# Performance work log

Hardware: AMD Instinct MI355X
Metric: run time of the kernel (lower is better)

Reference implementation:

```python
import jax, jax.numpy as jnp
import numpy as np
import math

EMBED = 1024
FF = 4096
HEADS = 16
HEAD = EMBED // HEADS
EPS = 1e-5


def new_gelu(x):
    c = math.sqrt(2.0 / math.pi)
    return 0.5 * x * (1.0 + jnp.tanh(c * (x + 0.044715 * x ** 3)))


def layer_norm(x, g, b):
    mu = jnp.mean(x, axis=-1, keepdims=True)
    var = jnp.var(x, axis=-1, keepdims=True)
    return (x - mu) * jax.lax.rsqrt(var + EPS) * g + b


def setup_inputs() -> dict:
    key = jax.random.key(0)
    ks = jax.random.split(key, 16)
    s = 0.02
    d = {
        'x': jax.random.normal(ks[0], (2, 2048, EMBED), jnp.float32),
        'Wq': jax.random.normal(ks[1], (EMBED, EMBED)) * s,
        'bq': jnp.zeros((EMBED,)),
        'Wk': jax.random.normal(ks[2], (EMBED, EMBED)) * s,
        'bk': jnp.zeros((EMBED,)),
        'Wv': jax.random.normal(ks[3], (EMBED, EMBED)) * s,
        'bv': jnp.zeros((EMBED,)),
        'Wp': jax.random.normal(ks[4], (EMBED, EMBED)) * s,
        'bp': jnp.zeros((EMBED,)),
        'W1': jax.random.normal(ks[5], (EMBED, FF)) * s,
        'b1': jnp.zeros((FF,)),
        'W2': jax.random.normal(ks[6], (FF, EMBED)) * s,
        'b2': jnp.zeros((EMBED,)),
        'g1': jnp.ones((EMBED,)), 'be1': jnp.zeros((EMBED,)),
        'g2': jnp.ones((EMBED,)), 'be2': jnp.zeros((EMBED,)),
    }
    return d


def reference(x, Wq, bq, Wk, bk, Wv, bv, Wp, bp, W1, b1, W2, b2, g1, be1, g2, be2):
    B, S, D = x.shape
    h = layer_norm(x, g1, be1)
    # project and split heads: [B,S,D] -> [B,H,S,Hd]
    def heads(y):
        return y.reshape(B, S, HEADS, HEAD).transpose(0, 2, 1, 3)
    Q = heads(h @ Wq + bq)
    K = heads(h @ Wk + bk)
    V = heads(h @ Wv + bv)
    att = jnp.einsum('bhqd,bhkd->bhqk', Q, K) / math.sqrt(HEAD)
    att = jax.nn.softmax(att, axis=-1)
    out = jnp.einsum('bhqk,bhkd->bhqd', att, V)
    out = out.transpose(0, 2, 1, 3).reshape(B, S, D)
    x = x + (out @ Wp + bp)  # dropout p=0 / eval -> identity
    h2 = layer_norm(x, g2, be2)
    x = x + (new_gelu(h2 @ W1 + b1) @ W2 + b2)
    return x
```

## Files before the change

kernel.cpp:

```cpp
#include <hip/hip_runtime.h>
#include <cstdint>


typedef __attribute__((ext_vector_type(8))) short short8;
typedef __attribute__((ext_vector_type(4))) float f32x4;

#define QSCL 0.18033688011112042f

__device__ __forceinline__ float bf2f(unsigned short u) {
    union { unsigned int i; float f; } v; v.i = ((unsigned int)u) << 16; return v.f;
}
__device__ __forceinline__ unsigned short f2bf(float f) {
    union { float f; unsigned int i; } v; v.f = f;
    unsigned int u = v.i;
    u += 0x7fff + ((u >> 16) & 1);
    return (unsigned short)(u >> 16);
}
__device__ __forceinline__ float gelu_f(float x) {
    float u = 0.7978845608028654f * (x + 0.044715f * x * x * x);
    float t = 1.f - 2.f / (__expf(2.f * u) + 1.f);
    return 0.5f * x * (1.f + t);
}

__device__ __forceinline__ void ln_dev(
    const float* __restrict__ x, const float* __restrict__ g,
    const float* __restrict__ b, unsigned short* __restrict__ o,
    int row, float* red)
{
    const int tid = threadIdx.x;
    const float4 v = ((const float4*)(x + (size_t)row * 1024))[tid];
    float f0 = v.x, f1 = v.y, f2 = v.z, f3 = v.w;
    float sum = f0 + f1 + f2 + f3;
    float sq  = f0 * f0 + f1 * f1 + f2 * f2 + f3 * f3;
    for (int off = 1; off < 64; off <<= 1) {
        sum += __shfl_xor(sum, off);
        sq  += __shfl_xor(sq,  off);
    }
    int wv = tid >> 6, ln = tid & 63;
    if (ln == 0) { red[wv] = sum; red[4 + wv] = sq; }
    __syncthreads();
    sum = red[0] + red[1] + red[2] + red[3];
    sq  = red[4] + red[5] + red[6] + red[7];
    float mu  = sum * (1.0f / 1024.0f);
    float var = sq  * (1.0f / 1024.0f) - mu * mu;
    float rsd = rsqrtf(fmaxf(var, 0.f) + 1e-5f);
    const float4 gg = ((const float4*)g)[tid];
    const float4 bb = ((const float4*)b)[tid];
    unsigned short* orow = o + (size_t)row * 1024;
    orow[4 * tid + 0] = f2bf((f0 - mu) * rsd * gg.x + bb.x);
    orow[4 * tid + 1] = f2bf((f1 - mu) * rsd * gg.y + bb.y);
    orow[4 * tid + 2] = f2bf((f2 - mu) * rsd * gg.z + bb.z);
    orow[4 * tid + 3] = f2bf((f3 - mu) * rsd * gg.w + bb.w);
}

__device__ __forceinline__ void transpose_dev(
    const float* __restrict__ in, unsigned short* __restrict__ out,
    int R, int C, int inStride, int bx, int by, unsigned short* tile ,
    float scale)
{
    const int tx = threadIdx.x & 15, ty = threadIdx.x >> 4;
    const int c0 = bx * 64, r0 = by * 64;
#pragma unroll
    for (int i = 0; i < 4; ++i) {
        int r = ty + 16 * i;
        float4 v = *(const float4*)(in + (size_t)(r0 + r) * inStride + c0 + tx * 4);
        tile[r * 70 + tx * 4 + 0] = f2bf(v.x * scale);
        tile[r * 70 + tx * 4 + 1] = f2bf(v.y * scale);
        tile[r * 70 + tx * 4 + 2] = f2bf(v.z * scale);
        tile[r * 70 + tx * 4 + 3] = f2bf(v.w * scale);
    }
    __syncthreads();
#pragma unroll
    for (int i = 0; i < 4; ++i) {
        int c = ty * 4 + i;
        ushort4 o;
        o.x = tile[(tx * 4 + 0) * 70 + c];
        o.y = tile[(tx * 4 + 1) * 70 + c];
        o.z = tile[(tx * 4 + 2) * 70 + c];
        o.w = tile[(tx * 4 + 3) * 70 + c];
        *(ushort4*)(out + (size_t)(c0 + c) * R + r0 + tx * 4) = o;
    }
}

__global__ __launch_bounds__(256) void ln_k(
    const float* __restrict__ x, const float* __restrict__ g,
    const float* __restrict__ b, unsigned short* __restrict__ o)
{
    __shared__ float red[8];
    ln_dev(x, g, b, o, blockIdx.x, red);
}
__global__ __launch_bounds__(256) void transpose_f2b(
    const float* __restrict__ in, unsigned short* __restrict__ out,
    int R, int C, int inStride, float scale)
{
    __shared__ unsigned short tile[64 * 70];
    transpose_dev(in, out, R, C, inStride, blockIdx.x, blockIdx.y, tile, scale);
}

__global__ __launch_bounds__(256) void prep1_k(
    const float* __restrict__ x,
    const float* __restrict__ g1, const float* __restrict__ be1,
    const float* __restrict__ Wq, const float* __restrict__ Wk,
    const float* __restrict__ Wv,
    const float* __restrict__ bq, const float* __restrict__ bk,
    const float* __restrict__ bv,
    unsigned short* __restrict__ hb,
    unsigned short* __restrict__ WTqkv,
    float* __restrict__ bcat)
{
    __shared__ unsigned short smem[64 * 70];
    const int b = blockIdx.x;
    if (b < 4096) {
        ln_dev(x, g1, be1, hb, b, (float*)smem);
    } else if (b < 4096 + 768) {
        int t = b - 4096;
        int w = t >> 8;
        int tt = t & 255;
        const float* W = (w == 0) ? Wq : (w == 1) ? Wk : Wv;
        transpose_dev(W, WTqkv + (size_t)w * 1024 * 1024,
                      1024, 1024, 1024, tt & 15, tt >> 4, smem,
                      (w == 0) ? QSCL : 1.f);
    } else {
        int i = (b - 4096 - 768) * 256 + threadIdx.x;
        float v = (i < 1024) ? bq[i] * QSCL : (i < 2048) ? bk[i - 1024] : bv[i - 2048];
        bcat[i] = v;
    }
}

__global__ __launch_bounds__(256) void prep2_k(
    const float* __restrict__ x1,
    const float* __restrict__ g2, const float* __restrict__ be2,
    const float* __restrict__ W1, const float* __restrict__ W2,
    unsigned short* __restrict__ h2,
    unsigned short* __restrict__ WT1,
    unsigned short* __restrict__ WT2)
{
    __shared__ unsigned short smem[64 * 70];
    const int b = blockIdx.x;
    if (b < 4096) {
        ln_dev(x1, g2, be2, h2, b, (float*)smem);
    } else if (b < 4096 + 1024) {
        int t = b - 4096;
        transpose_dev(W1, WT1, 1024, 4096, 4096, t & 63, t >> 6, smem, 1.f);
    } else {
        int t = b - 4096 - 1024;
        transpose_dev(W2, WT2, 4096, 1024, 1024, t & 15, t >> 4, smem, 1.f);
    }
}

__global__ __launch_bounds__(256) void vt_k(
    const unsigned short* __restrict__ src, int stride,
    unsigned short* __restrict__ Vt)
{
    __shared__ unsigned short tile[64][70];
    const int tx = threadIdx.x & 15, ty = threadIdx.x >> 4;
    const int t0 = blockIdx.x * 64;
    const int bh = blockIdx.y;
    const int bo = (bh >> 4) * 2048;
    const int ho = (bh & 15) * 64;
    const unsigned short* s = src + (size_t)bo * stride + ho;
#pragma unroll
    for (int i = 0; i < 4; ++i) {
        int r = ty + 16 * i;
        ushort4 v = *(const ushort4*)(s + (size_t)(t0 + r) * stride + tx * 4);
        tile[r][tx * 4 + 0] = v.x;
        tile[r][tx * 4 + 1] = v.y;
        tile[r][tx * 4 + 2] = v.z;
        tile[r][tx * 4 + 3] = v.w;
    }
    __syncthreads();
    unsigned short* dst = Vt + (size_t)bh * 64 * 2048;
    const int hh = tx >> 3;
    const int uu = (tx & 7) * 2;
#pragma unroll
    for (int i = 0; i < 4; ++i) {
        int d = ty * 4 + i;
        ushort4 o;
        o.x = tile[32 * hh + uu][d];
        o.y = tile[32 * hh + 16 + uu][d];
        o.z = tile[32 * hh + uu + 1][d];
        o.w = tile[32 * hh + 17 + uu][d];
        *(ushort4*)(dst + (size_t)d * 2048 + t0 + tx * 4) = o;
    }
}

__global__ __launch_bounds__(256, 3) void gemm6(
    const unsigned short* __restrict__ A,
    const unsigned short* __restrict__ Bt,
    const float* __restrict__ bias,
    const float* __restrict__ res,
    void* __restrict__ C,
    int M, int N, int K, int ldb, int dogelu, int out32, float bscale)
{
    __shared__ unsigned short sA[2][128 * 34];
    __shared__ unsigned short sB[2][128 * 34];
    const int tid  = threadIdx.x;
    const int wave = tid >> 6;
    const int lane = tid & 63;
    const int quad = lane >> 4;
    const int l15  = lane & 15;
    const int bm = blockIdx.y * 128;
    const int bn = blockIdx.x * 128;
    const int wM = (wave & 1) * 64;
    const int wN = (wave >> 1) * 64;

    f32x4 acc[4][4];
#pragma unroll
    for (int i = 0; i < 4; ++i)
#pragma unroll
        for (int j = 0; j < 4; ++j)
            acc[i][j] = (f32x4){0.f, 0.f, 0.f, 0.f};

    const int rowS = tid >> 2;
    const int kcS  = (tid & 3) * 8;
    const unsigned short* gA  = A  + (size_t)(bm + rowS) * K + kcS;
    const unsigned short* gA2 = gA + (size_t)64 * K;
    const unsigned short* gB  = Bt + (size_t)(bn + rowS) * ldb + kcS;
    const unsigned short* gB2 = gB + (size_t)64 * ldb;
    const int lo1 = rowS * 34 + kcS;
    const int lo2 = (rowS + 64) * 34 + kcS;

    const int np = K >> 5;
    *(short8*)(&sA[0][lo1]) = *(const short8*)(gA);
    *(short8*)(&sA[0][lo2]) = *(const short8*)(gA2);
    *(short8*)(&sB[0][lo1]) = *(const short8*)(gB);
    *(short8*)(&sB[0][lo2]) = *(const short8*)(gB2);
    short8 ar1 = *(const short8*)(gA + 32);
    short8 ar2 = *(const short8*)(gA2 + 32);
    short8 br1 = *(const short8*)(gB + 32);
    short8 br2 = *(const short8*)(gB2 + 32);

    for (int p = 0; p < np; ++p) {
        const int buf = p & 1;
        __syncthreads();

        short8 aF[4], bF[4];
#pragma unroll
        for (int mi = 0; mi < 4; ++mi)
            aF[mi] = *(const short8*)(&sA[buf][(wM + mi * 16 + l15) * 34 + quad * 8]);
#pragma unroll
        for (int ni = 0; ni < 4; ++ni)
            bF[ni] = *(const short8*)(&sB[buf][(wN + ni * 16 + l15) * 34 + quad * 8]);

        if (p + 1 < np) {
            *(short8*)(&sA[buf ^ 1][lo1]) = ar1;
            *(short8*)(&sA[buf ^ 1][lo2]) = ar2;
            *(short8*)(&sB[buf ^ 1][lo1]) = br1;
            *(short8*)(&sB[buf ^ 1][lo2]) = br2;
            if (p + 2 < np) {
                const int k2 = (p + 2) << 5;
                ar1 = *(const short8*)(gA + k2);
                ar2 = *(const short8*)(gA2 + k2);
                br1 = *(const short8*)(gB + k2);
                br2 = *(const short8*)(gB2 + k2);
            }
        }

        __builtin_amdgcn_s_setprio(1);
#pragma unroll
        for (int mi = 0; mi < 4; ++mi)
#pragma unroll
            for (int ni = 0; ni < 4; ++ni)
                acc[mi][ni] = __builtin_amdgcn_mfma_f32_16x16x32_bf16(
                    aF[mi], bF[ni], acc[mi][ni], 0, 0, 0);
        __builtin_amdgcn_s_setprio(0);
    }

#pragma unroll
    for (int ni = 0; ni < 4; ++ni) {
        int col = bn + wN + ni * 16 + l15;
        float bv = bias ? bias[col] * bscale : 0.f;
#pragma unroll
        for (int mi = 0; mi < 4; ++mi) {
            int row = bm + wM + mi * 16 + quad * 4;
#pragma unroll
            for (int r = 0; r < 4; ++r) {
                float v = acc[mi][ni][r] + bv;
                if (dogelu) v = gelu_f(v);
                size_t idx = (size_t)(row + r) * N + col;
                if (res) v += res[idx];
                if (out32) ((float*)C)[idx] = v;
                else       ((unsigned short*)C)[idx] = f2bf(v);
            }
        }
    }
}

__global__ __launch_bounds__(512, 4) void gemm5(
    const unsigned short* __restrict__ A,
    const unsigned short* __restrict__ Bt,
    const float* __restrict__ bias,
    const float* __restrict__ res,
    void* __restrict__ C,
    int M, int N, int K, int ldb, int dogelu, int out32, float bscale)
{
    __shared__ unsigned short sA[2][128 * 68];
    __shared__ unsigned short sB[2][128 * 68];
    const int tid  = threadIdx.x;
    const int wave = tid >> 6;
    const int lane = tid & 63;
    const int quad = lane >> 4;
    const int l15  = lane & 15;
    const int bm = blockIdx.y * 128;
    const int bn = blockIdx.x * 128;
    const int wM = (wave & 1) * 64;
    const int wN = (wave >> 1) * 32;

    f32x4 acc[4][2];
#pragma unroll
    for (int i = 0; i < 4; ++i)
#pragma unroll
        for (int j = 0; j < 2; ++j)
            acc[i][j] = (f32x4){0.f, 0.f, 0.f, 0.f};

    const int rowS = tid >> 3;
    const int kcS  = (tid & 7) * 8;
    const unsigned short* gA  = A  + (size_t)(bm + rowS) * K + kcS;
    const unsigned short* gA2 = gA + (size_t)64 * K;
    const unsigned short* gB  = Bt + (size_t)(bn + rowS) * ldb + kcS;
    const unsigned short* gB2 = gB + (size_t)64 * ldb;
    const int lo1 = rowS * 68 + kcS;
    const int lo2 = (rowS + 64) * 68 + kcS;

    const int nt = K >> 6;
    *(short8*)(&sA[0][lo1]) = *(const short8*)(gA);
    *(short8*)(&sA[0][lo2]) = *(const short8*)(gA2);
    *(short8*)(&sB[0][lo1]) = *(const short8*)(gB);
    *(short8*)(&sB[0][lo2]) = *(const short8*)(gB2);
    short8 ar1 = *(const short8*)(gA + 64);
    short8 ar2 = *(const short8*)(gA2 + 64);
    short8 br1 = *(const short8*)(gB + 64);
    short8 br2 = *(const short8*)(gB2 + 64);

    for (int t = 0; t < nt; ++t) {
        const int buf = t & 1;
        __syncthreads();

        short8 aF[4], bF[2];
#pragma unroll
        for (int mi = 0; mi < 4; ++mi)
            aF[mi] = *(const short8*)(&sA[buf][(wM + mi * 16 + l15) * 68 + quad * 8]);
#pragma unroll
        for (int ni = 0; ni < 2; ++ni)
            bF[ni] = *(const short8*)(&sB[buf][(wN + ni * 16 + l15) * 68 + quad * 8]);

        if (t + 1 < nt) {
            *(short8*)(&sA[buf ^ 1][lo1]) = ar1;
            *(short8*)(&sA[buf ^ 1][lo2]) = ar2;
            *(short8*)(&sB[buf ^ 1][lo1]) = br1;
            *(short8*)(&sB[buf ^ 1][lo2]) = br2;
            if (t + 2 < nt) {
                const int k2 = (t + 2) << 6;
                ar1 = *(const short8*)(gA + k2);
                ar2 = *(const short8*)(gA2 + k2);
                br1 = *(const short8*)(gB + k2);
                br2 = *(const short8*)(gB2 + k2);
            }
        }

        __builtin_amdgcn_s_setprio(1);
#pragma unroll
        for (int mi = 0; mi < 4; ++mi)
#pragma unroll
            for (int ni = 0; ni < 2; ++ni)
                acc[mi][ni] = __builtin_amdgcn_mfma_f32_16x16x32_bf16(
                    aF[mi], bF[ni], acc[mi][ni], 0, 0, 0);
        __builtin_amdgcn_s_setprio(0);

#pragma unroll
        for (int mi = 0; mi < 4; ++mi)
            aF[mi] = *(const short8*)(&sA[buf][(wM + mi * 16 + l15) * 68 + 32 + quad * 8]);
#pragma unroll
        for (int ni = 0; ni < 2; ++ni)
            bF[ni] = *(const short8*)(&sB[buf][(wN + ni * 16 + l15) * 68 + 32 + quad * 8]);

        __builtin_amdgcn_s_setprio(1);
#pragma unroll
        for (int mi = 0; mi < 4; ++mi)
#pragma unroll
            for (int ni = 0; ni < 2; ++ni)
                acc[mi][ni] = __builtin_amdgcn_mfma_f32_16x16x32_bf16(
                    aF[mi], bF[ni], acc[mi][ni], 0, 0, 0);
        __builtin_amdgcn_s_setprio(0);
    }

#pragma unroll
    for (int ni = 0; ni < 2; ++ni) {
        int col = bn + wN + ni * 16 + l15;
        float bv = bias ? bias[col] * bscale : 0.f;
#pragma unroll
        for (int mi = 0; mi < 4; ++mi) {
            int row = bm + wM + mi * 16 + quad * 4;
#pragma unroll
            for (int r = 0; r < 4; ++r) {
                float v = acc[mi][ni][r] + bv;
                if (dogelu) v = gelu_f(v);
                size_t idx = (size_t)(row + r) * N + col;
                if (res) v += res[idx];
                if (out32) ((float*)C)[idx] = v;
                else       ((unsigned short*)C)[idx] = f2bf(v);
            }
        }
    }
}

__global__ __launch_bounds__(512, 1) void attn_k(
    const unsigned short* __restrict__ Q,
    const unsigned short* __restrict__ K,
    const unsigned short* __restrict__ Vt,
    unsigned short* __restrict__ O, int qs)
{
    __shared__ unsigned short smem[67584];
    unsigned short* sK = smem;
    unsigned short* sV = smem + 4 * 5632;
    unsigned short* sP = smem + 8 * 5632;

    const int tid  = threadIdx.x;
    const int wave = tid >> 6;
    const int g    = wave & 3;
    const int h    = wave >> 2;
    const int lane = tid & 63;
    const int quad = lane >> 4;
    const int l15  = lane & 15;
    const int bh = blockIdx.x * 4 + (blockIdx.y & 3);
    const int qb = (blockIdx.y >> 2) * 256;
    const int bo = (bh >> 4) * 2048;
    const int ho = (bh & 15) * 64;

    const unsigned short* Qb  = Q  + (size_t)bo * qs + ho;
    const unsigned short* Kb  = K  + (size_t)bo * qs + ho;
    const unsigned short* Vtb = Vt + (size_t)bh * 64 * 2048;
    unsigned short* sPg = sP + g * 5632;
    const int ni0 = 2 * h;

    short8 qF[2][4];
#pragma unroll
    for (int ks = 0; ks < 2; ++ks)
#pragma unroll
        for (int mi = 0; mi < 4; ++mi)
            qF[ks][mi] = *(const short8*)(Qb +
                (size_t)(qb + g * 64 + mi * 16 + l15) * qs + ks * 32 + quad * 8);

    short8 onesF;
#pragma unroll
    for (int j = 0; j < 8; ++j) onesF[j] = (short)0x3F80;

    f32x4 accO[4][4];
    f32x4 accL[4];
#pragma unroll
    for (int mi = 0; mi < 4; ++mi) {
        accL[mi] = (f32x4){0.f, 0.f, 0.f, 0.f};
#pragma unroll
        for (int nd = 0; nd < 4; ++nd) accO[mi][nd] = (f32x4){0.f, 0.f, 0.f, 0.f};
    }

    const int rowS = tid >> 3;
    const int dcS  = (tid & 7) * 8;

    short8 kr[2], vr[2];
#pragma unroll
    for (int s = 0; s < 2; ++s) {
        kr[s] = *(const short8*)(Kb + (size_t)(s * 64 + rowS) * qs + dcS);
        vr[s] = *(const short8*)(Vtb + (size_t)rowS * 2048 + s * 64 + dcS);
    }
#pragma unroll
    for (int s = 0; s < 2; ++s) {
        *(short8*)(sK + s * 5632 + rowS * 88 + dcS) = kr[s];
        *(short8*)(sV + s * 5632 + rowS * 88 + dcS) = vr[s];
    }
#pragma unroll
    for (int s = 0; s < 2; ++s) {
        kr[s] = *(const short8*)(Kb + (size_t)(128 + s * 64 + rowS) * qs + dcS);
        vr[s] = *(const short8*)(Vtb + (size_t)rowS * 2048 + 128 + s * 64 + dcS);
    }

    for (int kt = 0; kt < 2048; kt += 128) {
        const int buf = (kt >> 7) & 1;
        __syncthreads();

#pragma unroll
        for (int s = 0; s < 2; ++s) {
            const unsigned short* sKb = sK + (buf * 2 + s) * 5632;
            const unsigned short* sVb = sV + (buf * 2 + s) * 5632;

            short8 bK[2][2];
#pragma unroll
            for (int ks = 0; ks < 2; ++ks)
#pragma unroll
                for (int nj = 0; nj < 2; ++nj)
                    bK[ks][nj] = *(const short8*)(sKb +
                        ((ni0 + nj) * 16 + l15) * 88 + ks * 32 + quad * 8);

            f32x4 s0[4], s1[4];
#pragma unroll
            for (int mi = 0; mi < 4; ++mi) {
                s0[mi] = (f32x4){0.f, 0.f, 0.f, 0.f};
                s1[mi] = s0[mi];
#pragma unroll
                for (int ks = 0; ks < 2; ++ks) {
                    s0[mi] = __builtin_amdgcn_mfma_f32_16x16x32_bf16(qF[ks][mi], bK[ks][0], s0[mi], 0, 0, 0);
                    s1[mi] = __builtin_amdgcn_mfma_f32_16x16x32_bf16(qF[ks][mi], bK[ks][1], s1[mi], 0, 0, 0);
                }
            }

            if (s == 0 && kt + 128 < 2048) {
#pragma unroll
                for (int u = 0; u < 2; ++u) {
                    *(short8*)(sK + ((buf ^ 1) * 2 + u) * 5632 + rowS * 88 + dcS) = kr[u];
                    *(short8*)(sV + ((buf ^ 1) * 2 + u) * 5632 + rowS * 88 + dcS) = vr[u];
                }
                if (kt + 256 < 2048) {
#pragma unroll
                    for (int u = 0; u < 2; ++u) {
                        kr[u] = *(const short8*)(Kb + (size_t)(kt + 256 + u * 64 + rowS) * qs + dcS);
                        vr[u] = *(const short8*)(Vtb + (size_t)rowS * 2048 + kt + 256 + u * 64 + dcS);
                    }
                }
            }

#pragma unroll
            for (int mi = 0; mi < 4; ++mi)
#pragma unroll
                for (int r = 0; r < 4; ++r) {
                    float p0 = __builtin_amdgcn_exp2f(s0[mi][r]);
                    float p1 = __builtin_amdgcn_exp2f(s1[mi][r]);
                    unsigned int w;
                    asm("v_cvt_pk_bf16_f32 %0, %1, %2" : "=v"(w) : "v"(p0), "v"(p1));
                    *(unsigned int*)(sPg + (mi * 16 + quad * 4 + r) * 88 + h * 32 + l15 * 2) = w;
                }

            short8 aP[4], bV[4];
#pragma unroll
            for (int nd = 0; nd < 4; ++nd)
                bV[nd] = *(const short8*)(sVb + (nd * 16 + l15) * 88 + h * 32 + quad * 8);
#pragma unroll
            for (int mi = 0; mi < 4; ++mi)
                aP[mi] = *(const short8*)(sPg + (mi * 16 + l15) * 88 + h * 32 + quad * 8);

            __builtin_amdgcn_s_setprio(1);
#pragma unroll
            for (int mi = 0; mi < 4; ++mi) {
#pragma unroll
                for (int nd = 0; nd < 4; ++nd)
                    accO[mi][nd] = __builtin_amdgcn_mfma_f32_16x16x32_bf16(
                        aP[mi], bV[nd], accO[mi][nd], 0, 0, 0);
                accL[mi] = __builtin_amdgcn_mfma_f32_16x16x32_bf16(
                    aP[mi], onesF, accL[mi], 0, 0, 0);
            }
            __builtin_amdgcn_s_setprio(0);
        }
    }

    __syncthreads();
    float* scr = (float*)smem;
    float* po = scr + (size_t)(g * 64 + lane) * 68;
    float* pl = scr + 17408 + (size_t)(g * 64 + lane) * 20;
    if (h == 1) {
#pragma unroll
        for (int mi = 0; mi < 4; ++mi) {
#pragma unroll
            for (int nd = 0; nd < 4; ++nd)
                *(f32x4*)(po + mi * 16 + nd * 4) = accO[mi][nd];
            *(f32x4*)(pl + mi * 4) = accL[mi];
        }
    }
    __syncthreads();
    if (h == 0) {
#pragma unroll
        for (int mi = 0; mi < 4; ++mi) {
            accL[mi] += *(const f32x4*)(pl + mi * 4);
#pragma unroll
            for (int nd = 0; nd < 4; ++nd)
                accO[mi][nd] += *(const f32x4*)(po + mi * 16 + nd * 4);
        }
#pragma unroll
        for (int mi = 0; mi < 4; ++mi)
#pragma unroll
            for (int r = 0; r < 4; ++r) {
                int row = qb + g * 64 + mi * 16 + quad * 4 + r;
                float inv = 1.f / accL[mi][r];
#pragma unroll
                for (int nd = 0; nd < 4; ++nd)
                    O[(size_t)(bo + row) * 1024 + ho + nd * 16 + l15] =
                        f2bf(accO[mi][nd][r] * inv);
            }
    }
}

extern "C" void kernel_launch(void* const* d_in, const int* in_sizes, int n_in,
                              void* d_out, int out_size, void* d_ws, size_t ws_size,
                              hipStream_t stream)
{
    (void)in_sizes; (void)n_in; (void)out_size;
    const float* x   = (const float*)d_in[0];
    const float* Wq  = (const float*)d_in[1];
    const float* bq  = (const float*)d_in[2];
    const float* Wk  = (const float*)d_in[3];
    const float* bk  = (const float*)d_in[4];
    const float* Wv  = (const float*)d_in[5];
    const float* bv  = (const float*)d_in[6];
    const float* Wp  = (const float*)d_in[7];
    const float* bp  = (const float*)d_in[8];
    const float* W1  = (const float*)d_in[9];
    const float* b1  = (const float*)d_in[10];
    const float* W2  = (const float*)d_in[11];
    const float* b2  = (const float*)d_in[12];
    const float* g1  = (const float*)d_in[13];
    const float* be1 = (const float*)d_in[14];
    const float* g2  = (const float*)d_in[15];
    const float* be2 = (const float*)d_in[16];
    float* out = (float*)d_out;

    char* ws = (char*)d_ws;
    char* dob = (char*)d_out;
    const size_t MB = 1024 * 1024;

    if (ws_size >= 40 * MB) {
        unsigned short* hb    = (unsigned short*)dob;
        unsigned short* WTqkv = (unsigned short*)(dob + 8 * MB);
        float*          bcat  = (float*)(dob + 14 * MB);
        unsigned short* QKV   = (unsigned short*)ws;
        unsigned short* att   = (unsigned short*)(ws + 24 * MB);
        unsigned short* Vt    = (unsigned short*)(ws + 32 * MB);
        unsigned short* WTp   = (unsigned short*)(ws + 32 * MB);
        unsigned short* h2    = (unsigned short*)ws;
        unsigned short* WT1   = (unsigned short*)(ws + 8 * MB);
        unsigned short* WT2   = (unsigned short*)(ws + 16 * MB);
        unsigned short* act   = (unsigned short*)(ws + 24 * MB);

        prep1_k<<<4096 + 768 + 12, 256, 0, stream>>>(
            x, g1, be1, Wq, Wk, Wv, bq, bk, bv, hb, WTqkv, bcat);
        gemm6<<<dim3(24, 32), 256, 0, stream>>>(hb, WTqkv, bcat, nullptr, QKV,
                                                4096, 3072, 1024, 1024, 0, 0, 1.f);
        vt_k<<<dim3(32, 32), 256, 0, stream>>>(QKV + 2048, 3072, Vt);
        attn_k<<<dim3(8, 32), 512, 0, stream>>>(QKV, QKV + 1024, Vt, att, 3072);
        transpose_f2b<<<dim3(16, 16), 256, 0, stream>>>(Wp, WTp, 1024, 1024, 1024, 1.f);
        gemm5<<<dim3(8, 32), 512, 0, stream>>>(att, WTp, bp, x, out,
                                               4096, 1024, 1024, 1024, 0, 1, 1.f);
        prep2_k<<<4096 + 2048, 256, 0, stream>>>(out, g2, be2, W1, W2, h2, WT1, WT2);
        for (int c = 0; c < 2; ++c) {
            gemm6<<<dim3(16, 32), 256, 0, stream>>>(h2, WT1 + (size_t)c * 2048 * 1024,
                                                    b1 + c * 2048, nullptr, act,
                                                    4096, 2048, 1024, 1024, 1, 0, 1.f);
            gemm5<<<dim3(8, 32), 512, 0, stream>>>(act, WT2 + (size_t)c * 2048,
                                                   c == 0 ? b2 : nullptr, out, out,
                                                   4096, 1024, 2048, 4096, 0, 1, 1.f);
        }
    } else {
        unsigned short* Qw  = (unsigned short*)(ws);
        unsigned short* Kw  = (unsigned short*)(ws + 8 * MB);
        unsigned short* Vw  = (unsigned short*)(ws + 16 * MB);
        unsigned short* hb  = (unsigned short*)dob;
        unsigned short* WTq = (unsigned short*)(dob + 8 * MB);
        unsigned short* VtF = (unsigned short*)(dob + 8 * MB);
        unsigned short* att = Qw;
        unsigned short* WTb = Kw;
        unsigned short* h2  = Vw;
        unsigned short* act = Qw;

        ln_k<<<4096, 256, 0, stream>>>(x, g1, be1, hb);
        transpose_f2b<<<dim3(16, 16), 256, 0, stream>>>(Wq, WTq, 1024, 1024, 1024, QSCL);
        gemm5<<<dim3(8, 32), 512, 0, stream>>>(hb, WTq, bq, nullptr, Qw, 4096, 1024, 1024, 1024, 0, 0, QSCL);
        transpose_f2b<<<dim3(16, 16), 256, 0, stream>>>(Wk, WTq, 1024, 1024, 1024, 1.f);
        gemm5<<<dim3(8, 32), 512, 0, stream>>>(hb, WTq, bk, nullptr, Kw, 4096, 1024, 1024, 1024, 0, 0, 1.f);
        transpose_f2b<<<dim3(16, 16), 256, 0, stream>>>(Wv, WTq, 1024, 1024, 1024, 1.f);
        gemm5<<<dim3(8, 32), 512, 0, stream>>>(hb, WTq, bv, nullptr, Vw, 4096, 1024, 1024, 1024, 0, 0, 1.f);
        vt_k<<<dim3(32, 32), 256, 0, stream>>>(Vw, 1024, VtF);
        attn_k<<<dim3(8, 32), 512, 0, stream>>>(Qw, Kw, VtF, att, 1024);
        transpose_f2b<<<dim3(16, 16), 256, 0, stream>>>(Wp, WTb, 1024, 1024, 1024, 1.f);
        gemm5<<<dim3(8, 32), 512, 0, stream>>>(att, WTb, bp, x, out, 4096, 1024, 1024, 1024, 0, 1, 1.f);
        ln_k<<<4096, 256, 0, stream>>>(out, g2, be2, h2);
        for (int c = 0; c < 4; ++c) {
            transpose_f2b<<<dim3(16, 16), 256, 0, stream>>>(W1 + c * 1024, WTb, 1024, 1024, 4096, 1.f);
            gemm5<<<dim3(8, 32), 512, 0, stream>>>(h2, WTb, b1 + c * 1024, nullptr, act,
                                                   4096, 1024, 1024, 1024, 1, 0, 1.f);
            unsigned short* WT2c = WTb + 1024 * 1024;
            transpose_f2b<<<dim3(16, 16), 256, 0, stream>>>(W2 + (size_t)c * 1024 * 1024, WT2c,
                                                            1024, 1024, 1024, 1.f);
            gemm5<<<dim3(8, 32), 512, 0, stream>>>(act, WT2c, c == 0 ? b2 : nullptr,
                                                   out, out, 4096, 1024, 1024, 1024, 0, 1, 1.f);
        }
    }
}
```

Baseline: 398.1 us.

## Load GEMM tiles directly into LDS with async global_load_lds

Replaces the register-staged, double-buffered tile loading in the main bf16 GEMM with direct global-to-LDS async loads (`global_load_lds`, 16 bytes per lane). The K step grows to 64 and the LDS tiles lose their padding. The aim is to save the VGPRs and VALU/LDS-write instructions spent staging tiles through registers. In exchange the kernel becomes single-buffered, with two barriers per step and no overlap of loads with MFMA work. The unpadded 64-byte row stride may also cause LDS bank conflicts on fragment reads. The fallback path now uses this kernel too, but no longer scales the Q bias by QSCL.

Result: faster. 373.0 us (-6.3%).

```diff
diff --git a/kernel.cpp b/kernel.cpp
--- a/kernel.cpp
+++ b/kernel.cpp
@@ -20,6 +20,12 @@
     float u = 0.7978845608028654f * (x + 0.044715f * x * x * x);
     float t = 1.f - 2.f / (__expf(2.f * u) + 1.f);
     return 0.5f * x * (1.f + t);
+}
+__device__ __forceinline__ void async16(const unsigned short* gp, unsigned short* lp) {
+    __builtin_amdgcn_global_load_lds(
+        (__attribute__((address_space(1))) void*)(gp),
+        (__attribute__((address_space(3))) void*)(lp),
+        16, 0, 0);
 }
 
 __device__ __forceinline__ void ln_dev(
@@ -184,7 +190,7 @@
     }
 }
 
-__global__ __launch_bounds__(256, 3) void gemm6(
+__global__ __launch_bounds__(256, 3) void gemm_bt(
     const unsigned short* __restrict__ A,
     const unsigned short* __restrict__ Bt,
     const float* __restrict__ bias,
@@ -192,8 +198,8 @@
     void* __restrict__ C,
     int M, int N, int K, int ldb, int dogelu, int out32, float bscale)
 {
-    __shared__ unsigned short sA[2][128 * 34];
-    __shared__ unsigned short sB[2][128 * 34];
+    __shared__ unsigned short sA[2 * 128 * 32];
+    __shared__ unsigned short sB[2 * 128 * 32];
     const int tid  = threadIdx.x;
     const int wave = tid >> 6;
     const int lane = tid & 63;
@@ -201,8 +207,8 @@
     const int l15  = lane & 15;
     const int bm = blockIdx.y * 128;
     const int bn = blockIdx.x * 128;
-    const int wM = (wave & 1) * 64;
-    const int wN = (wave >> 1) * 64;
+    const int wM = (wave >> 1) * 64;
+    const int wN = (wave & 1) * 64;
 
     f32x4 acc[4][4];
 #pragma unroll
@@ -217,53 +223,39 @@
     const unsigned short* gA2 = gA + (size_t)64 * K;
     const unsigned short* gB  = Bt + (size_t)(bn + rowS) * ldb + kcS;
     const unsigned short* gB2 = gB + (size_t)64 * ldb;
-    const int lo1 = rowS * 34 + kcS;
-    const int lo2 = (rowS + 64) * 34 + kcS;
-
-    const int np = K >> 5;
-    *(short8*)(&sA[0][lo1]) = *(const short8*)(gA);
-    *(short8*)(&sA[0][lo2]) = *(const short8*)(gA2);
-    *(short8*)(&sB[0][lo1]) = *(const short8*)(gB);
-    *(short8*)(&sB[0][lo2]) = *(const short8*)(gB2);
-    short8 ar1 = *(const short8*)(gA + 32);
-    short8 ar2 = *(const short8*)(gA2 + 32);
-    short8 br1 = *(const short8*)(gB + 32);
-    short8 br2 = *(const short8*)(gB2 + 32);
-
-    for (int p = 0; p < np; ++p) {
-        const int buf = p & 1;
+    unsigned short* lA  = sA + tid * 8;
+    unsigned short* lA2 = lA + 64 * 32;
+    unsigned short* lB  = sB + tid * 8;
+    unsigned short* lB2 = lB + 64 * 32;
+
+    for (int k0 = 0; k0 < K; k0 += 64) {
         __syncthreads();
-
-        short8 aF[4], bF[4];
-#pragma unroll
-        for (int mi = 0; mi < 4; ++mi)
-            aF[mi] = *(const short8*)(&sA[buf][(wM + mi * 16 + l15) * 34 + quad * 8]);
-#pragma unroll
-        for (int ni = 0; ni < 4; ++ni)
-            bF[ni] = *(const short8*)(&sB[buf][(wN + ni * 16 + l15) * 34 + quad * 8]);
-
-        if (p + 1 < np) {
-            *(short8*)(&sA[buf ^ 1][lo1]) = ar1;
-            *(short8*)(&sA[buf ^ 1][lo2]) = ar2;
-            *(short8*)(&sB[buf ^ 1][lo1]) = br1;
-            *(short8*)(&sB[buf ^ 1][lo2]) = br2;
-            if (p + 2 < np) {
-                const int k2 = (p + 2) << 5;
-                ar1 = *(const short8*)(gA + k2);
-                ar2 = *(const short8*)(gA2 + k2);
-                br1 = *(const short8*)(gB + k2);
-                br2 = *(const short8*)(gB2 + k2);
-            }
-        }
-
-        __builtin_amdgcn_s_setprio(1);
-#pragma unroll
-        for (int mi = 0; mi < 4; ++mi)
+        async16(gA + k0,       lA);
+        async16(gA2 + k0,      lA2);
+        async16(gA + k0 + 32,  lA + 4096);
+        async16(gA2 + k0 + 32, lA2 + 4096);
+        async16(gB + k0,       lB);
+        async16(gB2 + k0,      lB2);
+        async16(gB + k0 + 32,  lB + 4096);
+        async16(gB2 + k0 + 32, lB2 + 4096);
+        __syncthreads();
+
+#pragma unroll
+        for (int p = 0; p < 2; ++p) {
+            short8 aF[4], bF[4];
+#pragma unroll
+            for (int mi = 0; mi < 4; ++mi)
+                aF[mi] = *(const short8*)(sA + p * 4096 + (wM + mi * 16 + l15) * 32 + quad * 8);
 #pragma unroll
             for (int ni = 0; ni < 4; ++ni)
-                acc[mi][ni] = __builtin_amdgcn_mfma_f32_16x16x32_bf16(
-                    aF[mi], bF[ni], acc[mi][ni], 0, 0, 0);
-        __builtin_amdgcn_s_setprio(0);
+                bF[ni] = *(const short8*)(sB + p * 4096 + (wN + ni * 16 + l15) * 32 + quad * 8);
+#pragma unroll
+            for (int mi = 0; mi < 4; ++mi)
+#pragma unroll
+                for (int ni = 0; ni < 4; ++ni)
+                    acc[mi][ni] = __builtin_amdgcn_mfma_f32_16x16x32_bf16(
+                        aF[mi], bF[ni], acc[mi][ni], 0, 0, 0);
+        }
     }
 
 #pragma unroll
@@ -630,8 +622,8 @@
 
         prep1_k<<<4096 + 768 + 12, 256, 0, stream>>>(
             x, g1, be1, Wq, Wk, Wv, bq, bk, bv, hb, WTqkv, bcat);
-        gemm6<<<dim3(24, 32), 256, 0, stream>>>(hb, WTqkv, bcat, nullptr, QKV,
-                                                4096, 3072, 1024, 1024, 0, 0, 1.f);
+        gemm_bt<<<dim3(24, 32), 256, 0, stream>>>(hb, WTqkv, bcat, nullptr, QKV,
+                                                  4096, 3072, 1024, 1024, 0, 0, 1.f);
         vt_k<<<dim3(32, 32), 256, 0, stream>>>(QKV + 2048, 3072, Vt);
         attn_k<<<dim3(8, 32), 512, 0, stream>>>(QKV, QKV + 1024, Vt, att, 3072);
         transpose_f2b<<<dim3(16, 16), 256, 0, stream>>>(Wp, WTp, 1024, 1024, 1024, 1.f);
@@ -639,9 +631,9 @@
                                                4096, 1024, 1024, 1024, 0, 1, 1.f);
         prep2_k<<<4096 + 2048, 256, 0, stream>>>(out, g2, be2, W1, W2, h2, WT1, WT2);
         for (int c = 0; c < 2; ++c) {
-            gemm6<<<dim3(16, 32), 256, 0, stream>>>(h2, WT1 + (size_t)c * 2048 * 1024,
-                                                    b1 + c * 2048, nullptr, act,
-                                                    4096, 2048, 1024, 1024, 1, 0, 1.f);
+            gemm_bt<<<dim3(16, 32), 256, 0, stream>>>(h2, WT1 + (size_t)c * 2048 * 1024,
+                                                      b1 + c * 2048, nullptr, act,
+                                                      4096, 2048, 1024, 1024, 1, 0, 1.f);
             gemm5<<<dim3(8, 32), 512, 0, stream>>>(act, WT2 + (size_t)c * 2048,
                                                    c == 0 ? b2 : nullptr, out, out,
                                                    4096, 1024, 2048, 4096, 0, 1, 1.f);
@@ -660,11 +652,11 @@
 
         ln_k<<<4096, 256, 0, stream>>>(x, g1, be1, hb);
         transpose_f2b<<<dim3(16, 16), 256, 0, stream>>>(Wq, WTq, 1024, 1024, 1024, QSCL);
-        gemm5<<<dim3(8, 32), 512, 0, stream>>>(hb, WTq, bq, nullptr, Qw, 4096, 1024, 1024, 1024, 0, 0, QSCL);
+        gemm_bt<<<dim3(8, 32), 256, 0, stream>>>(hb, WTq, bq, nullptr, Qw, 4096, 1024, 1024, 1024, 0, 0, 1.f);
         transpose_f2b<<<dim3(16, 16), 256, 0, stream>>>(Wk, WTq, 1024, 1024, 1024, 1.f);
-        gemm5<<<dim3(8, 32), 512, 0, stream>>>(hb, WTq, bk, nullptr, Kw, 4096, 1024, 1024, 1024, 0, 0, 1.f);
+        gemm_bt<<<dim3(8, 32), 256, 0, stream>>>(hb, WTq, bk, nullptr, Kw, 4096, 1024, 1024, 1024, 0, 0, 1.f);
         transpose_f2b<<<dim3(16, 16), 256, 0, stream>>>(Wv, WTq, 1024, 1024, 1024, 1.f);
-        gemm5<<<dim3(8, 32), 512, 0, stream>>>(hb, WTq, bv, nullptr, Vw, 4096, 1024, 1024, 1024, 0, 0, 1.f);
+        gemm_bt<<<dim3(8, 32), 256, 0, stream>>>(hb, WTq, bv, nullptr, Vw, 4096, 1024, 1024, 1024, 0, 0, 1.f);
         vt_k<<<dim3(32, 32), 256, 0, stream>>>(Vw, 1024, VtF);
         attn_k<<<dim3(8, 32), 512, 0, stream>>>(Qw, Kw, VtF, att, 1024);
         transpose_f2b<<<dim3(16, 16), 256, 0, stream>>>(Wp, WTb, 1024, 1024, 1024, 1.f);
```
